# Performance work log

Measured on AMD Instinct MI355X. Metric: run time of the kernel, lower is better.

Reference implementation:

```python
import jax, jax.numpy as jnp
import numpy as np

B, N, C = 8, 4096, 256
HEADS, SR = 8, 4
LN_EPS = 1e-5

def setup_inputs() -> dict:
    key = jax.random.key(0)
    ks = jax.random.split(key, 8)
    std = 0.02
    x = jax.random.normal(ks[0], (B, N, C), dtype=jnp.float32)
    q_w = jax.random.normal(ks[1], (C, C), dtype=jnp.float32) * std          # [in,out]
    kv_w = jax.random.normal(ks[2], (C, 2 * C), dtype=jnp.float32) * std     # [in,2*out]
    fan_out = SR * SR * C
    sr_w = jax.random.normal(ks[3], (C, C, SR, SR), dtype=jnp.float32) * np.sqrt(2.0 / fan_out)  # OIHW
    sr_b = jnp.zeros((C,), dtype=jnp.float32)
    ln_w = jnp.ones((C,), dtype=jnp.float32)
    ln_b = jnp.zeros((C,), dtype=jnp.float32)
    proj_w = jax.random.normal(ks[4], (C, C), dtype=jnp.float32) * std
    proj_b = jnp.zeros((C,), dtype=jnp.float32)
    return {"x": x, "H": 64, "W": 64, "q_w": q_w, "kv_w": kv_w, "sr_w": sr_w,
            "sr_b": sr_b, "ln_w": ln_w, "ln_b": ln_b, "proj_w": proj_w, "proj_b": proj_b}


def reference(x, H, W, q_w, kv_w, sr_w, sr_b, ln_w, ln_b, proj_w, proj_b):
    Bb, Nn, Cc = x.shape
    hd = Cc // HEADS
    scale = hd ** -0.5
    # q: [B, heads, N, hd]
    q = (x @ q_w).reshape(Bb, Nn, HEADS, hd).transpose(0, 2, 1, 3)
    # spatial reduction: conv(stride=sr) + LayerNorm
    x_ = x.transpose(0, 2, 1).reshape(Bb, Cc, H, W)
    x_ = jax.lax.conv_general_dilated(
        x_, sr_w, window_strides=(SR, SR), padding="VALID",
        dimension_numbers=("NCHW", "OIHW", "NCHW")) + sr_b[None, :, None, None]
    x_ = x_.reshape(Bb, Cc, -1).transpose(0, 2, 1)  # [B, Nk, C]
    mu = x_.mean(-1, keepdims=True)
    var = x_.var(-1, keepdims=True)
    x_ = (x_ - mu) * jax.lax.rsqrt(var + LN_EPS) * ln_w + ln_b
    # kv: [B, Nk, 2, heads, hd]
    Nk = x_.shape[1]
    kv = (x_ @ kv_w).reshape(Bb, Nk, 2, HEADS, hd)
    k = kv[:, :, 0].transpose(0, 2, 1, 3)  # [B, heads, Nk, hd]
    v = kv[:, :, 1].transpose(0, 2, 1, 3)  # [B, heads, Nk, hd]
    attn = jnp.einsum("bhnd,bhmd->bhnm", q, k) * scale
    attn = jax.nn.softmax(attn, axis=-1)
    out = jnp.einsum("bhnm,bhmd->bhnd", attn, v)  # [B, heads, N, hd]
    out = out.transpose(0, 2, 1, 3).reshape(Bb, Nn, Cc)
    return out @ proj_w + proj_b
```

## Files before the change

### kernel.cpp

```cpp
#include <hip/hip_runtime.h>
#include <hip/hip_bf16.h>
#include <math.h>

#define DI __device__ __forceinline__

static constexpr float SCALE = 0.17677669529663687f;

typedef short bf16x8 __attribute__((ext_vector_type(8)));
typedef float f32x4 __attribute__((ext_vector_type(4)));

__device__ unsigned short g_qw2[(size_t)256 * 8 * 64];
__device__ unsigned short g_kvw2[(size_t)512 * 8 * 64];
__device__ unsigned short g_pw2[(size_t)256 * 8 * 64];
__device__ unsigned short g_wt2[(size_t)256 * 128 * 64];
__device__ unsigned short g_x2[(size_t)32768 * 8 * 64];
__device__ unsigned short g_ln2[(size_t)2048 * 8 * 64];
__device__ unsigned short g_q[(size_t)64 * 4096 * 32];
__device__ unsigned short g_k[(size_t)64 * 256 * 32];
__device__ unsigned short g_vt[(size_t)64 * 32 * 256];
__device__ unsigned short g_convp[(size_t)16 * 2048 * 256];
__device__ unsigned short g_attnb[(size_t)32768 * 256];

DI float bfbits2f(unsigned short b) { return __uint_as_float(((unsigned)b) << 16); }

DI unsigned short f2bf(float f) {
  unsigned u = __float_as_uint(f);
  unsigned r = (u + 0x7fffu + ((u >> 16) & 1u)) >> 16;
  return (unsigned short)r;
}

DI float4 ld_bf4(const unsigned short* p) {
  ushort4 u = *(const ushort4*)p;
  return make_float4(bfbits2f(u.x), bfbits2f(u.y), bfbits2f(u.z), bfbits2f(u.w));
}

DI float ld1(const void* p, size_t i, int f32) {
  return f32 ? ((const float*)p)[i] : bfbits2f(((const unsigned short*)p)[i]);
}

DI float4 ld4(const void* p, size_t i, int f32) {
  if (f32) return *(const float4*)((const float*)p + i);
  return ld_bf4((const unsigned short*)p + i);
}

typedef const __attribute__((address_space(1))) void* gas_p;
typedef __attribute__((address_space(3))) void* las_p;
DI void gload16(const unsigned short* g, short* l) {
  __builtin_amdgcn_global_load_lds((gas_p)g, (las_p)l, 16, 0, 0);
}

template <int N> DI void wait_vmcnt() {
  if constexpr (N == 6) asm volatile("s_waitcnt vmcnt(6)" ::: "memory");
  else if constexpr (N == 5) asm volatile("s_waitcnt vmcnt(5)" ::: "memory");
  else if constexpr (N == 4) asm volatile("s_waitcnt vmcnt(4)" ::: "memory");
  else asm volatile("s_waitcnt vmcnt(0)" ::: "memory");
}

DI int detect_f32(const void* xp) {
  const unsigned* p = (const unsigned*)xp;
  unsigned m0 = 0, m1 = 0;
#pragma unroll
  for (int i = 0; i < 32; ++i) {
    unsigned w = p[i];
    unsigned lo = w & 0x7fffu, hi = (w >> 16) & 0x7fffu;
    m0 = lo > m0 ? lo : m0;
    m1 = hi > m1 ? hi : m1;
  }
  unsigned mm = m0 > m1 ? m0 : m1;
  return mm >= 0x4680u ? 1 : 0;
}

__global__ void k_prep(const void* __restrict__ qw, const void* __restrict__ kvw,
                       const void* __restrict__ pwp, const void* __restrict__ srw,
                       const void* __restrict__ xp) {
  const int f32 = detect_f32(xp);
  int tidg = blockIdx.x * 256 + threadIdx.x;
  float v[8];
  unsigned short* dst;
  if (tidg < 8192) {
    int o = tidg >> 5, w = tidg & 31, k = w * 8;
#pragma unroll
    for (int j = 0; j < 8; ++j) v[j] = ld1(qw, (size_t)(k + j) * 256 + o, f32) * SCALE;
    dst = g_qw2 + ((size_t)o * 8 + (w >> 2)) * 64 + (w & 3) * 8;
  } else if (tidg < 24576) {
    int t = tidg - 8192;
    int o = t >> 5, w = t & 31, k = w * 8;
#pragma unroll
    for (int j = 0; j < 8; ++j) v[j] = ld1(kvw, (size_t)(k + j) * 512 + o, f32);
    dst = g_kvw2 + ((size_t)o * 8 + (w >> 2)) * 64 + (w & 3) * 8;
  } else if (tidg < 32768) {
    int t = tidg - 24576;
    int o = t >> 5, w = t & 31, k = w * 8;
#pragma unroll
    for (int j = 0; j < 8; ++j) v[j] = ld1(pwp, (size_t)(k + j) * 256 + o, f32);
    dst = g_pw2 + ((size_t)o * 8 + (w >> 2)) * 64 + (w & 3) * 8;
  } else if (tidg < 163840) {
    int t = tidg - 32768;
    int o = t >> 9, w = t & 511, k = w * 8;
#pragma unroll
    for (int j = 0; j < 8; ++j) {
      int kk = k + j, tap = kk >> 8, ci = kk & 255;
      v[j] = ld1(srw, (size_t)o * 4096 + (size_t)ci * 16 + tap, f32);
    }
    dst = g_wt2 + ((size_t)o * 128 + (w >> 2)) * 64 + (w & 3) * 8;
  } else {
    int t = tidg - 163840;
    int m = t >> 5, w = t & 31, k = w * 8;
    size_t base = (size_t)m * 256 + k;
    float4 a = ld4(xp, base, f32);
    float4 b = ld4(xp, base + 4, f32);
    v[0] = a.x; v[1] = a.y; v[2] = a.z; v[3] = a.w;
    v[4] = b.x; v[5] = b.y; v[6] = b.z; v[7] = b.w;
    dst = g_x2 + ((size_t)m * 8 + (w >> 2)) * 64 + (w & 3) * 8;
  }
  ushort4 h0, h1, l0, l1;
  h0.x = f2bf(v[0]); l0.x = f2bf(v[0] - bfbits2f(h0.x));
  h0.y = f2bf(v[1]); l0.y = f2bf(v[1] - bfbits2f(h0.y));
  h0.z = f2bf(v[2]); l0.z = f2bf(v[2] - bfbits2f(h0.z));
  h0.w = f2bf(v[3]); l0.w = f2bf(v[3] - bfbits2f(h0.w));
  h1.x = f2bf(v[4]); l1.x = f2bf(v[4] - bfbits2f(h1.x));
  h1.y = f2bf(v[5]); l1.y = f2bf(v[5] - bfbits2f(h1.y));
  h1.z = f2bf(v[6]); l1.z = f2bf(v[6] - bfbits2f(h1.z));
  h1.w = f2bf(v[7]); l1.w = f2bf(v[7] - bfbits2f(h1.w));
  *(ushort4*)dst        = h0;
  *(ushort4*)(dst + 4)  = h1;
  *(ushort4*)(dst + 32) = l0;
  *(ushort4*)(dst + 36) = l1;
}

template <int MODE>
DI void mgemm_body(short* smem, int bx, int nblk, int z,
                   const void* __restrict__ biasp, void* __restrict__ outp, int f32) {
  constexpr bool AH = (MODE != 3);
  constexpr int BN  = (MODE == 2) ? 64 : 128;
  constexpr int NJ  = BN / 64;
  constexpr int NBR = BN / 32;
  constexpr int ASZ = AH ? 4096 : 2048;
  constexpr int BSZ = NBR * 2048;
  constexpr int BUF = ASZ + BSZ;
  constexpr int NLD = (AH ? 2 : 1) + NBR;
  constexpr int NIT = (MODE == 1) ? 32 : 8;
  constexpr int NKT = (MODE == 1) ? 128 : 8;

  const int tid = threadIdx.x;
  const int m0 = bx * 64;
  const int wave = tid >> 6, lane = tid & 63;
  const int quad = lane >> 4, l15 = lane & 15;

  const int srow = tid >> 3;
  const int slot = (tid & 7) ^ (srow & 7);

  size_t arow0 = 0, arow1 = 0, abase3 = 0;
  if constexpr (MODE == 0 || MODE == 2) {
    arow0 = m0 + srow;
    arow1 = m0 + 32 + srow;
  } else if constexpr (MODE == 1) {
#pragma unroll
    for (int r = 0; r < 2; ++r) {
      int m = m0 + r * 32 + srow;
      int bb = m >> 8, sp = m & 255;
      int oh = sp >> 4, ow = sp & 15;
      size_t rb = (size_t)bb * 4096 + (4 * oh + z) * 64 + 4 * ow;
      if (r == 0) arow0 = rb; else arow1 = rb;
    }
  } else {
    int ar = tid >> 2;
    int s3 = (tid & 3) ^ (ar & 3);
    abase3 = (size_t)(m0 + ar) * 256 + s3 * 8;
  }

  const unsigned short* Asrc =
      (MODE == 0 || MODE == 1) ? g_x2 : (MODE == 2) ? g_ln2 : g_attnb;
  const unsigned short* Bsrc = (MODE == 0) ? g_qw2 : (MODE == 1) ? g_wt2
                             : (MODE == 2) ? g_kvw2 : g_pw2;
  const int brow0 = nblk * BN + srow;

  int aoff[4], boff[NJ];
#pragma unroll
  for (int mt = 0; mt < 4; ++mt) {
    int ar = mt * 16 + l15;
    if constexpr (AH) aoff[mt] = ar * 64 + ((quad ^ (ar & 7)) << 3);
    else              aoff[mt] = ar * 32 + ((quad ^ (ar & 3)) << 3);
  }
#pragma unroll
  for (int j = 0; j < NJ; ++j) {
    int br = wave * (16 * NJ) + j * 16 + l15;
    boff[j] = br * 64 + ((quad ^ (br & 7)) << 3);
  }

  auto STAGE = [&](int it, int b) {
    short* sa = smem + b * BUF;
    short* sb = sa + ASZ;
    if constexpr (MODE == 0 || MODE == 2) {
      gload16(Asrc + (arow0 * 8 + it) * 64 + slot * 8, sa + tid * 8);
      gload16(Asrc + (arow1 * 8 + it) * 64 + slot * 8, sa + 2048 + tid * 8);
    } else if constexpr (MODE == 1) {
      const int kw = it >> 3, ktA = it & 7;
      gload16(Asrc + ((arow0 + kw) * 8 + ktA) * 64 + slot * 8, sa + tid * 8);
      gload16(Asrc + ((arow1 + kw) * 8 + ktA) * 64 + slot * 8, sa + 2048 + tid * 8);
    } else {
      gload16(Asrc + abase3 + (size_t)it * 32, sa + tid * 8);
    }
    const int ktB = (MODE == 1) ? (z * 32 + it) : it;
#pragma unroll
    for (int r = 0; r < NBR; ++r)
      gload16(Bsrc + ((size_t)(brow0 + r * 32) * NKT + ktB) * 64 + slot * 8,
              sb + tid * 8 + r * 2048);
  };

  f32x4 acc[4][NJ] = {};

  auto COMPUTE = [&](int cur) {
    const short* sa = smem + cur * BUF;
    const short* sb = sa + ASZ;
#pragma unroll
    for (int mt = 0; mt < 4; ++mt) {
      bf16x8 a_h = *(const bf16x8*)&sa[aoff[mt]];
      bf16x8 a_l;
      if constexpr (AH) a_l = *(const bf16x8*)&sa[aoff[mt] ^ 32];
#pragma unroll
      for (int j = 0; j < NJ; ++j) {
        bf16x8 b_h = *(const bf16x8*)&sb[boff[j]];
        bf16x8 b_l = *(const bf16x8*)&sb[boff[j] ^ 32];
        f32x4 c = acc[mt][j];
        c = __builtin_amdgcn_mfma_f32_16x16x32_bf16(a_h, b_h, c, 0, 0, 0);
        if constexpr (AH)
          c = __builtin_amdgcn_mfma_f32_16x16x32_bf16(a_l, b_h, c, 0, 0, 0);
        c = __builtin_amdgcn_mfma_f32_16x16x32_bf16(a_h, b_l, c, 0, 0, 0);
        acc[mt][j] = c;
      }
    }
  };

  STAGE(0, 0);
  STAGE(1, 1);
#pragma unroll 1
  for (int it = 0; it < NIT - 1; ++it) {
    const int cur = it & 1;
    wait_vmcnt<NLD>();
    __builtin_amdgcn_s_barrier();
    __builtin_amdgcn_sched_barrier(0);
    COMPUTE(cur);
    asm volatile("" ::: "memory");
    __builtin_amdgcn_s_barrier();
    __builtin_amdgcn_sched_barrier(0);
    if (it < NIT - 2) STAGE(it + 2, cur);
  }
  wait_vmcnt<0>();
  __builtin_amdgcn_s_barrier();
  __builtin_amdgcn_sched_barrier(0);
  COMPUTE((NIT - 1) & 1);

  const int f32o = f32;
#pragma unroll
  for (int mt = 0; mt < 4; ++mt) {
#pragma unroll
    for (int j = 0; j < NJ; ++j) {
#pragma unroll
      for (int r = 0; r < 4; ++r) {
        int m = m0 + mt * 16 + quad * 4 + r;
        int c = nblk * BN + wave * (16 * NJ) + j * 16 + l15;
        float v = acc[mt][j][r];
        if constexpr (MODE == 0) {
          int b = m >> 12, n = m & 4095;
          int h = c >> 5, d = c & 31;
          g_q[(((size_t)(b * 8 + h) * 4096 + n) << 5) + d] = f2bf(v);
        } else if constexpr (MODE == 1) {
          g_convp[((size_t)z * 2048 + m) * 256 + c] = f2bf(v);
        } else if constexpr (MODE == 2) {
          int s = c >> 8, h = (c >> 5) & 7, d = c & 31;
          int bb = m >> 8, nk = m & 255;
          if (s == 0) {
            g_k[(((size_t)(bb * 8 + h) * 256 + nk) << 5) + d] = f2bf(v);
          } else {
            int w = nk & 31, cb = nk & ~31;
            int ww = w & 15;
            int vslot = cb + ((ww >> 2) << 3) + ((w >> 4) << 2) + (ww & 3);
            g_vt[(((size_t)(bb * 8 + h) * 32 + d) << 8) + vslot] = f2bf(v);
          }
        } else {
          float rr = v + ld1(biasp, c, f32o);
          if (f32o) ((float*)outp)[(size_t)m * 256 + c] = rr;
          else      ((unsigned short*)outp)[(size_t)m * 256 + c] = f2bf(rr);
        }
      }
    }
  }
}

__launch_bounds__(256, 3)
__global__ void k_mgemm01() {
  __shared__ __align__(16) short smem[2 * 12288];
  int bid = blockIdx.x;
  if (bid < 256) {
    int m = bid & 31, nb = (bid >> 5) & 1, z = bid >> 6;
    mgemm_body<1>(smem, m, nb, z, nullptr, nullptr, 0);
  } else {
    int bq = bid - 256;
    int lq = (bq & 7) * 128 + (bq >> 3);
    mgemm_body<0>(smem, lq >> 1, lq & 1, 0, nullptr, nullptr, 0);
  }
}

__launch_bounds__(256, 3)
__global__ void k_mgemm2() {
  __shared__ __align__(16) short smem[2 * 8192];
  int b = blockIdx.x;
  int lq = (b & 7) * 32 + (b >> 3);
  mgemm_body<2>(smem, lq >> 3, lq & 7, 0, nullptr, nullptr, 0);
}

__global__ void k_redln(const void* __restrict__ xp, const void* __restrict__ srb,
                        const void* __restrict__ lw, const void* __restrict__ lb) {
  const int f32 = detect_f32(xp);
  const int t = threadIdx.x;
  const int row = blockIdx.x * 8 + (t >> 5);
  const int l32 = t & 31;
  const int ch0 = l32 * 8;
  const size_t idx = (size_t)row * 256 + ch0;

  float c[8] = {};
#pragma unroll
  for (int zz = 0; zz < 4; ++zz) {
    uint4 u = *(const uint4*)&g_convp[(size_t)zz * (2048 * 256) + idx];
    c[0] += __uint_as_float(u.x << 16); c[1] += __uint_as_float(u.x & 0xffff0000u);
    c[2] += __uint_as_float(u.y << 16); c[3] += __uint_as_float(u.y & 0xffff0000u);
    c[4] += __uint_as_float(u.z << 16); c[5] += __uint_as_float(u.z & 0xffff0000u);
    c[6] += __uint_as_float(u.w << 16); c[7] += __uint_as_float(u.w & 0xffff0000u);
  }
  float4 b0 = ld4(srb, ch0, f32), b1 = ld4(srb, ch0 + 4, f32);
  c[0] += b0.x; c[1] += b0.y; c[2] += b0.z; c[3] += b0.w;
  c[4] += b1.x; c[5] += b1.y; c[6] += b1.z; c[7] += b1.w;

  float s = 0.f, sq = 0.f;
#pragma unroll
  for (int j = 0; j < 8; ++j) { s += c[j]; sq += c[j] * c[j]; }
#pragma unroll
  for (int off = 16; off >= 1; off >>= 1) {
    s += __shfl_xor(s, off, 32);
    sq += __shfl_xor(sq, off, 32);
  }
  float mu = s * (1.0f / 256.0f);
  float var = sq * (1.0f / 256.0f) - mu * mu;
  float rr = rsqrtf(var + 1e-5f);

  float4 w0 = ld4(lw, ch0, f32), w1 = ld4(lw, ch0 + 4, f32);
  float4 e0 = ld4(lb, ch0, f32), e1 = ld4(lb, ch0 + 4, f32);
  float wv[8] = {w0.x, w0.y, w0.z, w0.w, w1.x, w1.y, w1.z, w1.w};
  float ev[8] = {e0.x, e0.y, e0.z, e0.w, e1.x, e1.y, e1.z, e1.w};

  float o[8];
#pragma unroll
  for (int j = 0; j < 8; ++j) o[j] = (c[j] - mu) * rr * wv[j] + ev[j];

  ushort4 h0, h1, l0, l1;
  h0.x = f2bf(o[0]); l0.x = f2bf(o[0] - bfbits2f(h0.x));
  h0.y = f2bf(o[1]); l0.y = f2bf(o[1] - bfbits2f(h0.y));
  h0.z = f2bf(o[2]); l0.z = f2bf(o[2] - bfbits2f(h0.z));
  h0.w = f2bf(o[3]); l0.w = f2bf(o[3] - bfbits2f(h0.w));
  h1.x = f2bf(o[4]); l1.x = f2bf(o[4] - bfbits2f(h1.x));
  h1.y = f2bf(o[5]); l1.y = f2bf(o[5] - bfbits2f(h1.y));
  h1.z = f2bf(o[6]); l1.z = f2bf(o[6] - bfbits2f(h1.z));
  h1.w = f2bf(o[7]); l1.w = f2bf(o[7] - bfbits2f(h1.w));

  const size_t dbase = ((size_t)row * 8 + (l32 >> 2)) * 64 + (l32 & 3) * 8;
  *(ushort4*)&g_ln2[dbase]          = h0;
  *(ushort4*)&g_ln2[dbase + 4]      = h1;
  *(ushort4*)&g_ln2[dbase + 32]     = l0;
  *(ushort4*)&g_ln2[dbase + 36]     = l1;
}

__launch_bounds__(256, 2)
__global__ void k_attnproj(const void* __restrict__ xp, const void* __restrict__ pb,
                           void* __restrict__ outp) {
  __shared__ __align__(16) short smem[16384 + 18688];
  short* att = smem;
  short* skv = smem + 16384;

  const int f32o = detect_f32(xp);
  const int tid = threadIdx.x;
  int lq = ((int)blockIdx.x & 7) * 64 + ((int)blockIdx.x >> 3);
  const int b = lq >> 6, ntile = lq & 63;

  const int wave = tid >> 6, lane = tid & 63;
  const int quad = lane >> 4, l15 = lane & 15;
  const int rw = wave * 16 + l15;
  const int n0g = ntile * 64 + wave * 16;

  short* sk  = skv;
  short* svt = skv + 10240;

  {
    const uint4* gk = (const uint4*)(g_k + (size_t)(b * 8) * 8192);
    const uint4* gv = (const uint4*)(g_vt + (size_t)(b * 8) * 8192);
    for (int i = tid; i < 1024; i += 256) {
      int key = i >> 2, part = i & 3;
      *(uint4*)&sk[key * 40 + part * 8] = gk[i];
      int d = i >> 5, off = (i & 31) * 8;
      *(uint4*)&svt[d * 264 + off] = gv[i];
    }
  }
  __syncthreads();

  bf16x8 qv = *(const bf16x8*)(g_q + ((size_t)(b * 8) * 4096 + n0g + l15) * 32 + quad * 8);

#pragma unroll 1
  for (int h = 0; h < 8; ++h) {
    const int bh = b * 8 + h;

    f32x4 sacc[16];
    __builtin_amdgcn_s_setprio(1);
#pragma unroll
    for (int t = 0; t < 16; ++t) {
      bf16x8 kf = *(const bf16x8*)&sk[(t * 16 + l15) * 40 + quad * 8];
      f32x4 c = {0.f, 0.f, 0.f, 0.f};
      sacc[t] = __builtin_amdgcn_mfma_f32_16x16x32_bf16(kf, qv, c, 0, 0, 0);
    }
    __builtin_amdgcn_s_setprio(0);

    uint4 kreg0, kreg1, kreg2, kreg3, vreg0, vreg1, vreg2, vreg3;
    bf16x8 qvn;
    if (h < 7) {
      const uint4* gk = (const uint4*)(g_k + (size_t)(bh + 1) * 8192);
      const uint4* gv = (const uint4*)(g_vt + (size_t)(bh + 1) * 8192);
      kreg0 = gk[tid];       vreg0 = gv[tid];
      kreg1 = gk[tid + 256]; vreg1 = gv[tid + 256];
      kreg2 = gk[tid + 512]; vreg2 = gv[tid + 512];
      kreg3 = gk[tid + 768]; vreg3 = gv[tid + 768];
      qvn = *(const bf16x8*)(g_q + ((size_t)(bh + 1) * 4096 + n0g + l15) * 32 + quad * 8);
    }

    float m = sacc[0][0];
#pragma unroll
    for (int t = 0; t < 16; ++t) {
#pragma unroll
      for (int r = 0; r < 4; ++r) m = fmaxf(m, sacc[t][r]);
    }
    m = fmaxf(m, __shfl_xor(m, 16, 64));
    m = fmaxf(m, __shfl_xor(m, 32, 64));

    unsigned plo[16], phi[16];
    float ls = 0.f;
#pragma unroll
    for (int t = 0; t < 16; ++t) {
      unsigned short p0 = f2bf(__expf(sacc[t][0] - m));
      unsigned short p1 = f2bf(__expf(sacc[t][1] - m));
      unsigned short p2 = f2bf(__expf(sacc[t][2] - m));
      unsigned short p3 = f2bf(__expf(sacc[t][3] - m));
      ls += bfbits2f(p0) + bfbits2f(p1) + bfbits2f(p2) + bfbits2f(p3);
      plo[t] = (unsigned)p0 | ((unsigned)p1 << 16);
      phi[t] = (unsigned)p2 | ((unsigned)p3 << 16);
    }
    ls += __shfl_xor(ls, 16, 64);
    ls += __shfl_xor(ls, 32, 64);
    float inv = 1.0f / ls;

    f32x4 o0 = {0.f, 0.f, 0.f, 0.f}, o1 = {0.f, 0.f, 0.f, 0.f};
    __builtin_amdgcn_s_setprio(1);
#pragma unroll
    for (int c = 0; c < 8; ++c) {
      uint4 pk = make_uint4(plo[2 * c], phi[2 * c], plo[2 * c + 1], phi[2 * c + 1]);
      bf16x8 pf = *(bf16x8*)&pk;
      bf16x8 v0 = *(const bf16x8*)&svt[l15 * 264 + c * 32 + quad * 8];
      bf16x8 v1 = *(const bf16x8*)&svt[(16 + l15) * 264 + c * 32 + quad * 8];
      o0 = __builtin_amdgcn_mfma_f32_16x16x32_bf16(v0, pf, o0, 0, 0, 0);
      o1 = __builtin_amdgcn_mfma_f32_16x16x32_bf16(v1, pf, o1, 0, 0, 0);
    }
    __builtin_amdgcn_s_setprio(0);

    ushort4 u0, u1;
    u0.x = f2bf(o0[0] * inv); u0.y = f2bf(o0[1] * inv);
    u0.z = f2bf(o0[2] * inv); u0.w = f2bf(o0[3] * inv);
    u1.x = f2bf(o1[0] * inv); u1.y = f2bf(o1[1] * inv);
    u1.z = f2bf(o1[2] * inv); u1.w = f2bf(o1[3] * inv);
    int s0 = h * 4 + (quad >> 1);
    int woff = (quad & 1) * 4;
    *(ushort4*)&att[rw * 256 + (((s0    ) ^ (rw & 7)) << 3) + woff] = u0;
    *(ushort4*)&att[rw * 256 + (((s0 + 2) ^ (rw & 7)) << 3) + woff] = u1;

    if (h < 7) {
      __syncthreads();
      {
        int key = tid >> 2, part = tid & 3;
        *(uint4*)&sk[key * 40 + part * 8] = kreg0;
        int key1 = (tid + 256) >> 2;
        *(uint4*)&sk[key1 * 40 + part * 8] = kreg1;
        int key2 = (tid + 512) >> 2;
        *(uint4*)&sk[key2 * 40 + part * 8] = kreg2;
        int key3 = (tid + 768) >> 2;
        *(uint4*)&sk[key3 * 40 + part * 8] = kreg3;
        int d0 = tid >> 5, off = (tid & 31) * 8;
        *(uint4*)&svt[d0 * 264 + off] = vreg0;
        *(uint4*)&svt[(d0 + 8) * 264 + off] = vreg1;
        *(uint4*)&svt[(d0 + 16) * 264 + off] = vreg2;
        *(uint4*)&svt[(d0 + 24) * 264 + off] = vreg3;
      }
      qv = qvn;
      __syncthreads();
    } else {
      __syncthreads();
    }
  }

  const int srow = tid >> 3;
  const int slot = (tid & 7) ^ (srow & 7);

  auto STAGE_B = [&](int s) {
    short* sb = skv + (s & 1) * 8192;
    int nb = s >> 3, it = s & 7;
    int brow0 = nb * 128 + srow;
#pragma unroll
    for (int r = 0; r < 4; ++r)
      gload16(g_pw2 + ((size_t)(brow0 + r * 32) * 8 + it) * 64 + slot * 8,
              sb + tid * 8 + r * 2048);
  };

  int boff[2];
#pragma unroll
  for (int j = 0; j < 2; ++j) {
    int br = wave * 32 + j * 16 + l15;
    boff[j] = br * 64 + ((quad ^ (br & 7)) << 3);
  }

  f32x4 accA[4][2] = {};
  f32x4 accB[4][2] = {};

  auto PCOMP = [&](f32x4 (&acc)[4][2], int s) {
    const short* sb = skv + (s & 1) * 8192;
    int it = s & 7;
#pragma unroll
    for (int mt = 0; mt < 4; ++mt) {
      int ar = mt * 16 + l15;
      bf16x8 a_h = *(const bf16x8*)&att[ar * 256 + (((it * 4 + quad) ^ (ar & 7)) << 3)];
#pragma unroll
      for (int j = 0; j < 2; ++j) {
        bf16x8 b_h = *(const bf16x8*)&sb[boff[j]];
        bf16x8 b_l = *(const bf16x8*)&sb[boff[j] ^ 32];
        f32x4 c = acc[mt][j];
        c = __builtin_amdgcn_mfma_f32_16x16x32_bf16(a_h, b_h, c, 0, 0, 0);
        c = __builtin_amdgcn_mfma_f32_16x16x32_bf16(a_h, b_l, c, 0, 0, 0);
        acc[mt][j] = c;
      }
    }
  };

  STAGE_B(0);
  STAGE_B(1);
#pragma unroll 1
  for (int s = 0; s < 8; ++s) {
    wait_vmcnt<4>();
    __builtin_amdgcn_s_barrier();
    __builtin_amdgcn_sched_barrier(0);
    PCOMP(accA, s);
    asm volatile("" ::: "memory");
    __builtin_amdgcn_s_barrier();
    __builtin_amdgcn_sched_barrier(0);
    STAGE_B(s + 2);
  }
#pragma unroll 1
  for (int s = 8; s < 15; ++s) {
    wait_vmcnt<4>();
    __builtin_amdgcn_s_barrier();
    __builtin_amdgcn_sched_barrier(0);
    PCOMP(accB, s);
    asm volatile("" ::: "memory");
    __builtin_amdgcn_s_barrier();
    __builtin_amdgcn_sched_barrier(0);
    if (s < 14) STAGE_B(s + 2);
  }
  wait_vmcnt<0>();
  __builtin_amdgcn_s_barrier();
  __builtin_amdgcn_sched_barrier(0);
  PCOMP(accB, 15);

#pragma unroll
  for (int nb = 0; nb < 2; ++nb) {
#pragma unroll
    for (int mt = 0; mt < 4; ++mt) {
#pragma unroll
      for (int j = 0; j < 2; ++j) {
#pragma unroll
        for (int r = 0; r < 4; ++r) {
          int m = ntile * 64 + mt * 16 + quad * 4 + r;
          int c = nb * 128 + wave * 32 + j * 16 + l15;
          float v = (nb == 0 ? accA[mt][j][r] : accB[mt][j][r]) + ld1(pb, c, f32o);
          if (f32o) ((float*)outp)[((size_t)b * 4096 + m) * 256 + c] = v;
          else ((unsigned short*)outp)[((size_t)b * 4096 + m) * 256 + c] = f2bf(v);
        }
      }
    }
  }
}

extern "C" void kernel_launch(void* const* d_in, const int* in_sizes, int n_in,
                              void* d_out, int out_size, void* d_ws, size_t ws_size,
                              hipStream_t stream) {
  const void* x   = d_in[0];
  const void* qw  = d_in[3];
  const void* kvw = d_in[4];
  const void* srw = d_in[5];
  const void* srb = d_in[6];
  const void* lnw = d_in[7];
  const void* lnb = d_in[8];
  const void* pw  = d_in[9];
  const void* pb  = d_in[10];

  k_prep<<<4736, 256, 0, stream>>>(qw, kvw, pw, srw, x);
  k_mgemm01<<<1280, 256, 0, stream>>>();
  k_redln<<<256, 256, 0, stream>>>(x, srb, lnw, lnb);
  k_mgemm2<<<256, 256, 0, stream>>>();
  k_attnproj<<<512, 256, 0, stream>>>(x, pb, d_out);
}
```

Before: 199.3 us.

## Fuse conv-partial reduction and LayerNorm into the KV GEMM kernel

```diff
diff --git a/kernel.cpp b/kernel.cpp
--- a/kernel.cpp
+++ b/kernel.cpp
@@ -53,6 +53,7 @@
   if constexpr (N == 6) asm volatile("s_waitcnt vmcnt(6)" ::: "memory");
   else if constexpr (N == 5) asm volatile("s_waitcnt vmcnt(5)" ::: "memory");
   else if constexpr (N == 4) asm volatile("s_waitcnt vmcnt(4)" ::: "memory");
+  else if constexpr (N == 2) asm volatile("s_waitcnt vmcnt(2)" ::: "memory");
   else asm volatile("s_waitcnt vmcnt(0)" ::: "memory");
 }
 
@@ -302,72 +303,159 @@
   }
 }
 
-__launch_bounds__(256, 3)
-__global__ void k_mgemm2() {
-  __shared__ __align__(16) short smem[2 * 8192];
-  int b = blockIdx.x;
-  int lq = (b & 7) * 32 + (b >> 3);
-  mgemm_body<2>(smem, lq >> 3, lq & 7, 0, nullptr, nullptr, 0);
-}
-
-__global__ void k_redln(const void* __restrict__ xp, const void* __restrict__ srb,
-                        const void* __restrict__ lw, const void* __restrict__ lb) {
+__launch_bounds__(256, 2)
+__global__ void k_mgemm2(const void* __restrict__ xp, const void* __restrict__ srb,
+                         const void* __restrict__ lw, const void* __restrict__ lb) {
+  __shared__ __align__(16) short smem[32768 + 8192];
+  short* sa = smem;
+  short* sb = smem + 32768;
+
   const int f32 = detect_f32(xp);
-  const int t = threadIdx.x;
-  const int row = blockIdx.x * 8 + (t >> 5);
-  const int l32 = t & 31;
-  const int ch0 = l32 * 8;
-  const size_t idx = (size_t)row * 256 + ch0;
-
-  float c[8] = {};
-#pragma unroll
-  for (int zz = 0; zz < 4; ++zz) {
-    uint4 u = *(const uint4*)&g_convp[(size_t)zz * (2048 * 256) + idx];
-    c[0] += __uint_as_float(u.x << 16); c[1] += __uint_as_float(u.x & 0xffff0000u);
-    c[2] += __uint_as_float(u.y << 16); c[3] += __uint_as_float(u.y & 0xffff0000u);
-    c[4] += __uint_as_float(u.z << 16); c[5] += __uint_as_float(u.z & 0xffff0000u);
-    c[6] += __uint_as_float(u.w << 16); c[7] += __uint_as_float(u.w & 0xffff0000u);
-  }
-  float4 b0 = ld4(srb, ch0, f32), b1 = ld4(srb, ch0 + 4, f32);
-  c[0] += b0.x; c[1] += b0.y; c[2] += b0.z; c[3] += b0.w;
-  c[4] += b1.x; c[5] += b1.y; c[6] += b1.z; c[7] += b1.w;
-
-  float s = 0.f, sq = 0.f;
-#pragma unroll
-  for (int j = 0; j < 8; ++j) { s += c[j]; sq += c[j] * c[j]; }
-#pragma unroll
-  for (int off = 16; off >= 1; off >>= 1) {
-    s += __shfl_xor(s, off, 32);
-    sq += __shfl_xor(sq, off, 32);
-  }
-  float mu = s * (1.0f / 256.0f);
-  float var = sq * (1.0f / 256.0f) - mu * mu;
-  float rr = rsqrtf(var + 1e-5f);
-
-  float4 w0 = ld4(lw, ch0, f32), w1 = ld4(lw, ch0 + 4, f32);
-  float4 e0 = ld4(lb, ch0, f32), e1 = ld4(lb, ch0 + 4, f32);
-  float wv[8] = {w0.x, w0.y, w0.z, w0.w, w1.x, w1.y, w1.z, w1.w};
-  float ev[8] = {e0.x, e0.y, e0.z, e0.w, e1.x, e1.y, e1.z, e1.w};
-
-  float o[8];
-#pragma unroll
-  for (int j = 0; j < 8; ++j) o[j] = (c[j] - mu) * rr * wv[j] + ev[j];
-
-  ushort4 h0, h1, l0, l1;
-  h0.x = f2bf(o[0]); l0.x = f2bf(o[0] - bfbits2f(h0.x));
-  h0.y = f2bf(o[1]); l0.y = f2bf(o[1] - bfbits2f(h0.y));
-  h0.z = f2bf(o[2]); l0.z = f2bf(o[2] - bfbits2f(h0.z));
-  h0.w = f2bf(o[3]); l0.w = f2bf(o[3] - bfbits2f(h0.w));
-  h1.x = f2bf(o[4]); l1.x = f2bf(o[4] - bfbits2f(h1.x));
-  h1.y = f2bf(o[5]); l1.y = f2bf(o[5] - bfbits2f(h1.y));
-  h1.z = f2bf(o[6]); l1.z = f2bf(o[6] - bfbits2f(h1.z));
-  h1.w = f2bf(o[7]); l1.w = f2bf(o[7] - bfbits2f(h1.w));
-
-  const size_t dbase = ((size_t)row * 8 + (l32 >> 2)) * 64 + (l32 & 3) * 8;
-  *(ushort4*)&g_ln2[dbase]          = h0;
-  *(ushort4*)&g_ln2[dbase + 4]      = h1;
-  *(ushort4*)&g_ln2[dbase + 32]     = l0;
-  *(ushort4*)&g_ln2[dbase + 36]     = l1;
+  const int tid = threadIdx.x;
+  int lq = ((int)blockIdx.x & 7) * 32 + ((int)blockIdx.x >> 3);
+  const int bx = lq >> 3, nblk = lq & 7;
+  const int m0 = bx * 64;
+
+  const int wave = tid >> 6, lane = tid & 63;
+  const int quad = lane >> 4, l15 = lane & 15;
+  const int srow = tid >> 3;
+  const int slot = (tid & 7) ^ (srow & 7);
+  const int brow0 = nblk * 64 + srow;
+
+  auto STAGE_B = [&](int it) {
+    short* p = sb + (it & 1) * 4096;
+#pragma unroll
+    for (int r = 0; r < 2; ++r)
+      gload16(g_kvw2 + ((size_t)(brow0 + r * 32) * 8 + it) * 64 + slot * 8,
+              p + tid * 8 + r * 2048);
+  };
+  STAGE_B(0);
+  STAGE_B(1);
+
+  {
+    const int l32 = tid & 31;
+    const int ch0 = l32 * 8;
+    const int w = l32 & 3, kt = l32 >> 2;
+    float4 b0 = ld4(srb, ch0, f32), b1 = ld4(srb, ch0 + 4, f32);
+    float4 w0 = ld4(lw, ch0, f32), w1 = ld4(lw, ch0 + 4, f32);
+    float4 e0 = ld4(lb, ch0, f32), e1 = ld4(lb, ch0 + 4, f32);
+    float bv[8] = {b0.x, b0.y, b0.z, b0.w, b1.x, b1.y, b1.z, b1.w};
+    float wv[8] = {w0.x, w0.y, w0.z, w0.w, w1.x, w1.y, w1.z, w1.w};
+    float ev[8] = {e0.x, e0.y, e0.z, e0.w, e1.x, e1.y, e1.z, e1.w};
+#pragma unroll 1
+    for (int pass = 0; pass < 8; ++pass) {
+      const int row = pass * 8 + (tid >> 5);
+      const size_t idx = (size_t)(m0 + row) * 256 + ch0;
+      float c[8] = {};
+#pragma unroll
+      for (int zz = 0; zz < 4; ++zz) {
+        uint4 u = *(const uint4*)&g_convp[(size_t)zz * (2048 * 256) + idx];
+        c[0] += __uint_as_float(u.x << 16); c[1] += __uint_as_float(u.x & 0xffff0000u);
+        c[2] += __uint_as_float(u.y << 16); c[3] += __uint_as_float(u.y & 0xffff0000u);
+        c[4] += __uint_as_float(u.z << 16); c[5] += __uint_as_float(u.z & 0xffff0000u);
+        c[6] += __uint_as_float(u.w << 16); c[7] += __uint_as_float(u.w & 0xffff0000u);
+      }
+#pragma unroll
+      for (int j = 0; j < 8; ++j) c[j] += bv[j];
+      float s = 0.f, sq = 0.f;
+#pragma unroll
+      for (int j = 0; j < 8; ++j) { s += c[j]; sq += c[j] * c[j]; }
+#pragma unroll
+      for (int off = 16; off >= 1; off >>= 1) {
+        s += __shfl_xor(s, off, 32);
+        sq += __shfl_xor(sq, off, 32);
+      }
+      float mu = s * (1.0f / 256.0f);
+      float var = sq * (1.0f / 256.0f) - mu * mu;
+      float rr = rsqrtf(var + 1e-5f);
+      float o[8];
+#pragma unroll
+      for (int j = 0; j < 8; ++j) o[j] = (c[j] - mu) * rr * wv[j] + ev[j];
+
+      ushort4 h0, h1, l0, l1;
+      h0.x = f2bf(o[0]); l0.x = f2bf(o[0] - bfbits2f(h0.x));
+      h0.y = f2bf(o[1]); l0.y = f2bf(o[1] - bfbits2f(h0.y));
+      h0.z = f2bf(o[2]); l0.z = f2bf(o[2] - bfbits2f(h0.z));
+      h0.w = f2bf(o[3]); l0.w = f2bf(o[3] - bfbits2f(h0.w));
+      h1.x = f2bf(o[4]); l1.x = f2bf(o[4] - bfbits2f(h1.x));
+      h1.y = f2bf(o[5]); l1.y = f2bf(o[5] - bfbits2f(h1.y));
+      h1.z = f2bf(o[6]); l1.z = f2bf(o[6] - bfbits2f(h1.z));
+      h1.w = f2bf(o[7]); l1.w = f2bf(o[7] - bfbits2f(h1.w));
+
+      const int r7 = row & 7;
+      short* base = sa + row * 512 + kt * 64;
+      const int sh = (w ^ r7) << 3;
+      const int sl = sh ^ 32;
+      *(ushort4*)&base[sh]     = h0;
+      *(ushort4*)&base[sh + 4] = h1;
+      *(ushort4*)&base[sl]     = l0;
+      *(ushort4*)&base[sl + 4] = l1;
+    }
+  }
+  __syncthreads();
+
+  int aswz[4];
+#pragma unroll
+  for (int mt = 0; mt < 4; ++mt) {
+    int ar = mt * 16 + l15;
+    aswz[mt] = ar * 512 + ((quad ^ (ar & 7)) << 3);
+  }
+  const int br = wave * 16 + l15;
+  const int boff = br * 64 + ((quad ^ (br & 7)) << 3);
+
+  f32x4 acc[4] = {};
+  auto COMPUTE = [&](int it) {
+    const short* sp = sb + (it & 1) * 4096;
+#pragma unroll
+    for (int mt = 0; mt < 4; ++mt) {
+      int ao = aswz[mt] + it * 64;
+      bf16x8 a_h = *(const bf16x8*)&sa[ao];
+      bf16x8 a_l = *(const bf16x8*)&sa[ao ^ 32];
+      bf16x8 b_h = *(const bf16x8*)&sp[boff];
+      bf16x8 b_l = *(const bf16x8*)&sp[boff ^ 32];
+      f32x4 cc = acc[mt];
+      cc = __builtin_amdgcn_mfma_f32_16x16x32_bf16(a_h, b_h, cc, 0, 0, 0);
+      cc = __builtin_amdgcn_mfma_f32_16x16x32_bf16(a_l, b_h, cc, 0, 0, 0);
+      cc = __builtin_amdgcn_mfma_f32_16x16x32_bf16(a_h, b_l, cc, 0, 0, 0);
+      acc[mt] = cc;
+    }
+  };
+
+#pragma unroll 1
+  for (int it = 0; it < 7; ++it) {
+    wait_vmcnt<2>();
+    __builtin_amdgcn_s_barrier();
+    __builtin_amdgcn_sched_barrier(0);
+    COMPUTE(it);
+    asm volatile("" ::: "memory");
+    __builtin_amdgcn_s_barrier();
+    __builtin_amdgcn_sched_barrier(0);
+    if (it < 6) STAGE_B(it + 2);
+  }
+  wait_vmcnt<0>();
+  __builtin_amdgcn_s_barrier();
+  __builtin_amdgcn_sched_barrier(0);
+  COMPUTE(7);
+
+#pragma unroll
+  for (int mt = 0; mt < 4; ++mt) {
+#pragma unroll
+    for (int r = 0; r < 4; ++r) {
+      int m = m0 + mt * 16 + quad * 4 + r;
+      int c = nblk * 64 + wave * 16 + l15;
+      float v = acc[mt][r];
+      int s = c >> 8, h = (c >> 5) & 7, d = c & 31;
+      int bb = m >> 8, nk = m & 255;
+      if (s == 0) {
+        g_k[(((size_t)(bb * 8 + h) * 256 + nk) << 5) + d] = f2bf(v);
+      } else {
+        int w = nk & 31, cb = nk & ~31;
+        int ww = w & 15;
+        int vslot = cb + ((ww >> 2) << 3) + ((w >> 4) << 2) + (ww & 3);
+        g_vt[(((size_t)(bb * 8 + h) * 32 + d) << 8) + vslot] = f2bf(v);
+      }
+    }
+  }
 }
 
 __launch_bounds__(256, 2)
@@ -607,7 +695,6 @@
 
   k_prep<<<4736, 256, 0, stream>>>(qw, kvw, pw, srw, x);
   k_mgemm01<<<1280, 256, 0, stream>>>();
-  k_redln<<<256, 256, 0, stream>>>(x, srb, lnw, lnb);
-  k_mgemm2<<<256, 256, 0, stream>>>();
+  k_mgemm2<<<256, 256, 0, stream>>>(x, srb, lnw, lnb);
   k_attnproj<<<512, 256, 0, stream>>>(x, pb, d_out);
 }
```

After: 201.5 us. About the same (+1.1%).
